# Kernel optimization log

Hardware: AMD Instinct MI355X
Metric: run time of the kernel (lower is better)

## Reference

```python
import jax, jax.numpy as jnp
import numpy as np
from jax import lax

N = 512  # neurons (== input features in this base class)

@jax.custom_vjp
def spike_fn(x):
    # Heaviside spike with fast-sigmoid surrogate gradient (standard for LIF SNNs)
    return (x > 0.0).astype(x.dtype)

def _spike_fwd(x):
    return spike_fn(x), x

def _spike_bwd(x, g):
    sg = 1.0 / (1.0 + 10.0 * jnp.abs(x)) ** 2
    return (g * sg,)

spike_fn.defvjp(_spike_fwd, _spike_bwd)

def setup_inputs() -> dict:
    key = jax.random.key(0)
    k1, k2, k3, k4, k5, k6 = jax.random.split(key, 6)
    B, T = 64, 1000
    scale = 1.0 / np.sqrt(N)
    return {
        "input_batch": jax.random.normal(k1, (B, T, N), dtype=jnp.float32),
        "state_snn": jnp.zeros((2, B, N), dtype=jnp.float32),  # [v; s]
        "state_LI": jnp.zeros((B, N), dtype=jnp.float32),
        "W1": jax.random.normal(k2, (N, N), dtype=jnp.float32) * scale,
        "W2": jax.random.normal(k3, (N, N), dtype=jnp.float32) * scale,
        "leak_v": jax.random.uniform(k4, (N,), dtype=jnp.float32, minval=0.8, maxval=0.99),
        "leak_i": jax.random.uniform(k5, (N,), dtype=jnp.float32, minval=0.8, maxval=0.99),
        "thresh": jax.random.uniform(k6, (N,), dtype=jnp.float32, minval=0.5, maxval=1.5),
    }

def reference(input_batch, state_snn, state_LI, W1, W2, leak_v, leak_i, thresh):
    # input_batch: [B, T, N]; time loop expressed as lax.scan over T
    v0, s0 = state_snn[0], state_snn[1]
    xs = jnp.swapaxes(input_batch, 0, 1)  # [T, B, N]

    def step(carry, x_t):
        v, s, u = carry
        ff = x_t @ W1.T                        # LIF feed-forward current
        v = leak_v * v * (1.0 - s) + ff        # leak + reset-to-zero on spike
        s = spike_fn(v - thresh)               # spike generation
        u = leak_i * u + s @ W2.T              # leaky-integrator readout
        return (v, s, u), (s, jnp.stack([v, s]), u)

    _, (spikes, states_snn, decoded) = lax.scan(step, (v0, s0, state_LI), xs)
    # spikes: [T,B,N], states_snn: [T,2,B,N], decoded: [T,B,N]
    return spikes, states_snn, decoded
```

## Files before the change

### kernel.cpp

```cpp
#include <hip/hip_runtime.h>

#define T_STEPS 1000
#define B_SZ 64
#define N_SZ 512
#define BN_TOT (B_SZ * N_SZ)
#define TBN   ((size_t)T_STEPS * BN_TOT)

typedef __attribute__((ext_vector_type(4))) float f32x4;
typedef __attribute__((ext_vector_type(8))) short bf16x8;
typedef unsigned short ushort_t;

__global__ __launch_bounds__(256, 4)
void sgemm_abt(const float* __restrict__ A, const float* __restrict__ W,
               float* __restrict__ C)
{
    constexpr int K = 512;
    constexpr int BK = 16;
    constexpr int LDT = 128 + 4;
    __shared__ float As[BK][LDT];
    __shared__ float Bs[BK][LDT];

    const int tid = threadIdx.x;
    const int tx = tid & 15;
    const int ty = tid >> 4;
    const size_t m0 = (size_t)blockIdx.y * 128;
    const int n0 = blockIdx.x * 128;

    float acc[8][8];
#pragma unroll
    for (int i = 0; i < 8; ++i)
#pragma unroll
        for (int j = 0; j < 8; ++j) acc[i][j] = 0.0f;

    for (int k0 = 0; k0 < K; k0 += BK) {
#pragma unroll
        for (int p = 0; p < 2; ++p) {
            int i = tid + p * 256;
            int r = i >> 2;
            int q = i & 3;
            float4 va = *(const float4*)(A + (m0 + r) * K + k0 + q * 4);
            As[q * 4 + 0][r] = va.x; As[q * 4 + 1][r] = va.y;
            As[q * 4 + 2][r] = va.z; As[q * 4 + 3][r] = va.w;
            float4 vb = *(const float4*)(W + (size_t)(n0 + r) * K + k0 + q * 4);
            Bs[q * 4 + 0][r] = vb.x; Bs[q * 4 + 1][r] = vb.y;
            Bs[q * 4 + 2][r] = vb.z; Bs[q * 4 + 3][r] = vb.w;
        }
        __syncthreads();
#pragma unroll
        for (int k = 0; k < BK; ++k) {
            float a[8], b[8];
            *(float4*)&a[0] = *(const float4*)&As[k][ty * 8];
            *(float4*)&a[4] = *(const float4*)&As[k][ty * 8 + 4];
            *(float4*)&b[0] = *(const float4*)&Bs[k][tx * 4];
            *(float4*)&b[4] = *(const float4*)&Bs[k][tx * 4 + 64];
#pragma unroll
            for (int i = 0; i < 8; ++i)
#pragma unroll
                for (int j = 0; j < 8; ++j)
                    acc[i][j] = fmaf(a[i], b[j], acc[i][j]);
        }
        __syncthreads();
    }

#pragma unroll
    for (int i = 0; i < 8; ++i) {
        float* cp = C + (m0 + ty * 8 + i) * 512 + n0 + tx * 4;
        *(float4*)cp        = make_float4(acc[i][0], acc[i][1], acc[i][2], acc[i][3]);
        *(float4*)(cp + 64) = make_float4(acc[i][4], acc[i][5], acc[i][6], acc[i][7]);
    }
}

__global__ __launch_bounds__(256)
void w2_split(const float* __restrict__ W2, ushort_t* __restrict__ Wc)
{
    int i = blockIdx.x * 256 + threadIdx.x;
    int n = i >> 9, k = i & 511;
    float w = W2[i];
    unsigned wb = __float_as_uint(w);
    float h = __uint_as_float(wb & 0xFFFF0000u);
    float r1 = w - h;
    unsigned r1b = __float_as_uint(r1);
    size_t base = (size_t)n * 1024 + k;
    Wc[base]       = (ushort_t)(wb >> 16);
    Wc[base + 512] = (ushort_t)(r1b >> 16);
}

__global__ __launch_bounds__(256, 2)
void gemm2_mfma(const ushort_t* __restrict__ S, const ushort_t* __restrict__ Wc,
                float* __restrict__ C)
{
    constexpr int NT = 1024 / 32;
    __shared__ ushort_t As[2][128 * 32];
    __shared__ ushort_t Bs[2][128 * 32];

    const int tid = threadIdx.x;
    const int m0 = blockIdx.y * 128;
    const int n0 = blockIdx.x * 128;
    const int wid = tid >> 6;
    const int lane = tid & 63;
    const int wm = (wid >> 1) * 64;
    const int wn = (wid & 1) * 64;
    const int fr = lane & 15;
    const int fq = lane >> 4;

    f32x4 acc[4][4] = {};

    const int rA = tid >> 2;
    const int cA = (tid & 3) * 8;

#define STAGE(buf, t)                                                        \
    {                                                                        \
        const int k0_ = (t) * 32;                                            \
        const int kk_ = k0_ & 511;         \
        _Pragma("unroll")                                                    \
        for (int i = 0; i < 2; ++i) {                                        \
            __builtin_amdgcn_global_load_lds(                                \
                (const __attribute__((address_space(1))) unsigned int*)      \
                    (S + (size_t)(m0 + i * 64 + rA) * 512 + kk_ + cA),       \
                (__attribute__((address_space(3))) unsigned int*)            \
                    (As[buf] + i * 2048 + tid * 8),                          \
                16, 0, 0);                                                   \
            __builtin_amdgcn_global_load_lds(                                \
                (const __attribute__((address_space(1))) unsigned int*)      \
                    (Wc + (size_t)(n0 + i * 64 + rA) * 1024 + k0_ + cA),     \
                (__attribute__((address_space(3))) unsigned int*)            \
                    (Bs[buf] + i * 2048 + tid * 8),                          \
                16, 0, 0);                                                   \
        }                                                                    \
    }

    STAGE(0, 0);
    asm volatile("s_waitcnt vmcnt(0)" ::: "memory");
    __syncthreads();

    int cur = 0;
    for (int t = 0; t < NT; ++t) {
        if (t + 1 < NT)
            STAGE(cur ^ 1, t + 1);

        bf16x8 a[4], b[4];
#pragma unroll
        for (int m = 0; m < 4; ++m)
            a[m] = *(const bf16x8*)(As[cur] + (wm + m * 16 + fr) * 32 + fq * 8);
#pragma unroll
        for (int n = 0; n < 4; ++n)
            b[n] = *(const bf16x8*)(Bs[cur] + (wn + n * 16 + fr) * 32 + fq * 8);
#pragma unroll
        for (int m = 0; m < 4; ++m)
#pragma unroll
            for (int n = 0; n < 4; ++n)
                acc[m][n] = __builtin_amdgcn_mfma_f32_16x16x32_bf16(
                    a[m], b[n], acc[m][n], 0, 0, 0);

        asm volatile("s_waitcnt vmcnt(0)" ::: "memory");
        __syncthreads();
        cur ^= 1;
    }
#undef STAGE

#pragma unroll
    for (int m = 0; m < 4; ++m) {
        const int row = m0 + wm + m * 16 + fq * 4;
#pragma unroll
        for (int n = 0; n < 4; ++n) {
            const int col = n0 + wn + n * 16 + fr;
#pragma unroll
            for (int j = 0; j < 4; ++j)
                C[(size_t)(row + j) * 512 + col] = acc[m][n][j];
        }
    }
}

__global__ __launch_bounds__(128)
void lif_scan(const float* __restrict__ ff, const float* __restrict__ st0,
              const float* __restrict__ leak_v, const float* __restrict__ thresh,
              float* __restrict__ spikes, float* __restrict__ states,
              ushort_t* __restrict__ sbf)
{
    const int idx = blockIdx.x * 128 + threadIdx.x;
    const int n = idx & (N_SZ - 1);
    const int b = idx >> 9;

    float v = st0[idx];
    float s = st0[BN_TOT + idx];
    const float lv = leak_v[n];
    const float th = thresh[n];

    const float* fp = ff + (size_t)b * T_STEPS * N_SZ + n;
    float* sp  = spikes + idx;
    float* stp = states + idx;
    ushort_t* sbp = sbf ? (sbf + idx) : (ushort_t*)0;

    float f0 = fp[0], f1 = fp[N_SZ], f2 = fp[2 * N_SZ], f3 = fp[3 * N_SZ];

    for (int t = 0; t < T_STEPS; t += 4) {
        float g0 = 0.f, g1 = 0.f, g2 = 0.f, g3 = 0.f;
        if (t + 4 < T_STEPS) {
            const float* q = fp + (size_t)(t + 4) * N_SZ;
            g0 = q[0]; g1 = q[N_SZ]; g2 = q[2 * N_SZ]; g3 = q[3 * N_SZ];
        }
#define LIF_STEP(F, TOFF)                                                  \
        {                                                                  \
            v = lv * v * (1.0f - s) + (F);                                 \
            s = (v > th) ? 1.0f : 0.0f;                                    \
            size_t o  = (size_t)(t + (TOFF)) * BN_TOT;                     \
            size_t o2 = (size_t)(t + (TOFF)) * (2 * BN_TOT);               \
            sp[o] = s;                                                     \
            stp[o2] = v;                                                   \
            stp[o2 + BN_TOT] = s;                                          \
            if (sbp) sbp[o] = (ushort_t)(__float_as_uint(s) >> 16);        \
        }
        LIF_STEP(f0, 0) LIF_STEP(f1, 1) LIF_STEP(f2, 2) LIF_STEP(f3, 3)
#undef LIF_STEP
        f0 = g0; f1 = g1; f2 = g2; f3 = g3;
    }
}

__global__ __launch_bounds__(128)
void li_scan(float* __restrict__ dec, const float* __restrict__ u0,
             const float* __restrict__ leak_i)
{
    const int idx = blockIdx.x * 128 + threadIdx.x;
    const int n = idx & (N_SZ - 1);

    float u = u0[idx];
    const float li = leak_i[n];
    float* p = dec + idx;

    float y0 = p[0], y1 = p[BN_TOT], y2 = p[2 * (size_t)BN_TOT], y3 = p[3 * (size_t)BN_TOT];

    for (int t = 0; t < T_STEPS; t += 4) {
        float g0 = 0.f, g1 = 0.f, g2 = 0.f, g3 = 0.f;
        if (t + 4 < T_STEPS) {
            float* q = p + (size_t)(t + 4) * BN_TOT;
            g0 = q[0]; g1 = q[BN_TOT]; g2 = q[2 * (size_t)BN_TOT]; g3 = q[3 * (size_t)BN_TOT];
        }
#define LI_STEP(Y, TOFF)                                                   \
        {                                                                  \
            u = fmaf(li, u, (Y));                                          \
            p[(size_t)(t + (TOFF)) * BN_TOT] = u;                          \
        }
        LI_STEP(y0, 0) LI_STEP(y1, 1) LI_STEP(y2, 2) LI_STEP(y3, 3)
#undef LI_STEP
        y0 = g0; y1 = g1; y2 = g2; y3 = g3;
    }
}

extern "C" void kernel_launch(void* const* d_in, const int* in_sizes, int n_in,
                              void* d_out, int out_size, void* d_ws, size_t ws_size,
                              hipStream_t stream)
{
    (void)in_sizes; (void)n_in; (void)out_size;

    const float* X     = (const float*)d_in[0];
    const float* st_sn = (const float*)d_in[1];
    const float* st_li = (const float*)d_in[2];
    const float* W1    = (const float*)d_in[3];
    const float* W2    = (const float*)d_in[4];
    const float* lv    = (const float*)d_in[5];
    const float* li    = (const float*)d_in[6];
    const float* th    = (const float*)d_in[7];

    float* spikes = (float*)d_out;
    float* states = spikes + TBN;
    float* dec    = states + 2 * TBN;

    const size_t WS_NEED = (size_t)512 * 1024 * 2 + (size_t)64000 * 512 * 2;
    const bool use_mfma = (ws_size >= WS_NEED);
    ushort_t* Wc = (ushort_t*)d_ws;
    ushort_t* Sb = Wc + (size_t)512 * 1024;

    const dim3 gemm_grid(4, 500), gemm_block(256);
    const dim3 scan_grid(BN_TOT / 128), scan_block(128);

    if (use_mfma)
        w2_split<<<dim3(1024), dim3(256), 0, stream>>>(W2, Wc);

    sgemm_abt<<<gemm_grid, gemm_block, 0, stream>>>(X, W1, dec);

    lif_scan<<<scan_grid, scan_block, 0, stream>>>(dec, st_sn, lv, th,
                                                   spikes, states,
                                                   use_mfma ? Sb : (ushort_t*)0);

    if (use_mfma)
        gemm2_mfma<<<gemm_grid, gemm_block, 0, stream>>>(Sb, Wc, dec);
    else
        sgemm_abt<<<gemm_grid, gemm_block, 0, stream>>>(spikes, W2, dec);

    li_scan<<<scan_grid, scan_block, 0, stream>>>(dec, st_li, li);
}
```

Before: 811.8 us.

## Pack spikes into ballot bitmasks and expand to bf16 in GEMM2 staging

The LIF scan no longer writes a per-element bf16 spike array. Instead it uses a wave ballot to write one 64-bit spike bitmask per wave per timestep. The MFMA GEMM reads these masks and expands each bit into a bf16 1.0/0 pair (high and low K halves) in registers, then stores that into shared memory in place of the async global-to-LDS copy of A. Both scans are also unrolled from 4 to 8 timesteps with deeper prefetch. This cuts the spike intermediate traffic about 16x, at the cost of ALU work, a ballot per step and synchronous LDS stores in the GEMM loop.

After: 732.3 us. -9.8%, faster.

```diff
diff --git a/kernel.cpp b/kernel.cpp
--- a/kernel.cpp
+++ b/kernel.cpp
@@ -85,8 +85,18 @@
     Wc[base + 512] = (ushort_t)(r1b >> 16);
 }
 
+__device__ __forceinline__ uint4 mexp8(unsigned bb)
+{
+    uint4 r;
+    r.x = ((bb) & 1u) * 0x3F80u        | (((bb) >> 1) & 1u) * 0x3F800000u;
+    r.y = (((bb) >> 2) & 1u) * 0x3F80u | (((bb) >> 3) & 1u) * 0x3F800000u;
+    r.z = (((bb) >> 4) & 1u) * 0x3F80u | (((bb) >> 5) & 1u) * 0x3F800000u;
+    r.w = (((bb) >> 6) & 1u) * 0x3F80u | (((bb) >> 7) & 1u) * 0x3F800000u;
+    return r;
+}
+
 __global__ __launch_bounds__(256, 2)
-void gemm2_mfma(const ushort_t* __restrict__ S, const ushort_t* __restrict__ Wc,
+void gemm2_mfma(const unsigned* __restrict__ Msk, const ushort_t* __restrict__ Wc,
                 float* __restrict__ C)
 {
     constexpr int NT = 1024 / 32;
@@ -107,19 +117,17 @@
 
     const int rA = tid >> 2;
     const int cA = (tid & 3) * 8;
-
-#define STAGE(buf, t)                                                        \
+    const size_t mrow0 = (size_t)(m0 + (tid >> 2)) * 16;
+    const size_t mrow1 = (size_t)(m0 + 64 + (tid >> 2)) * 16;
+    const int qsh = (tid & 3) * 8;
+
+    unsigned mw0, mw1;
+
+#define STAGE_B(buf, t)                                                      \
     {                                                                        \
         const int k0_ = (t) * 32;                                            \
-        const int kk_ = k0_ & 511;         \
         _Pragma("unroll")                                                    \
         for (int i = 0; i < 2; ++i) {                                        \
-            __builtin_amdgcn_global_load_lds(                                \
-                (const __attribute__((address_space(1))) unsigned int*)      \
-                    (S + (size_t)(m0 + i * 64 + rA) * 512 + kk_ + cA),       \
-                (__attribute__((address_space(3))) unsigned int*)            \
-                    (As[buf] + i * 2048 + tid * 8),                          \
-                16, 0, 0);                                                   \
             __builtin_amdgcn_global_load_lds(                                \
                 (const __attribute__((address_space(1))) unsigned int*)      \
                     (Wc + (size_t)(n0 + i * 64 + rA) * 1024 + k0_ + cA),     \
@@ -128,15 +136,30 @@
                 16, 0, 0);                                                   \
         }                                                                    \
     }
-
-    STAGE(0, 0);
+#define MLOAD(t)                                                             \
+    {                                                                        \
+        const int kk_ = ((t) * 32) & 511;       \
+        mw0 = Msk[mrow0 + (kk_ >> 5)];                                       \
+        mw1 = Msk[mrow1 + (kk_ >> 5)];                                       \
+    }
+#define MSTORE(buf)                                                          \
+    {                                                                        \
+        *(uint4*)(As[buf] + tid * 8)        = mexp8((mw0 >> qsh) & 0xFFu);   \
+        *(uint4*)(As[buf] + 2048 + tid * 8) = mexp8((mw1 >> qsh) & 0xFFu);   \
+    }
+
+    MLOAD(0);
+    STAGE_B(0, 0);
+    MSTORE(0);
     asm volatile("s_waitcnt vmcnt(0)" ::: "memory");
     __syncthreads();
 
     int cur = 0;
     for (int t = 0; t < NT; ++t) {
-        if (t + 1 < NT)
-            STAGE(cur ^ 1, t + 1);
+        if (t + 1 < NT) {
+            MLOAD(t + 1);
+            STAGE_B(cur ^ 1, t + 1);
+        }
 
         bf16x8 a[4], b[4];
 #pragma unroll
@@ -152,11 +175,16 @@
                 acc[m][n] = __builtin_amdgcn_mfma_f32_16x16x32_bf16(
                     a[m], b[n], acc[m][n], 0, 0, 0);
 
+        if (t + 1 < NT)
+            MSTORE(cur ^ 1);
+
         asm volatile("s_waitcnt vmcnt(0)" ::: "memory");
         __syncthreads();
         cur ^= 1;
     }
-#undef STAGE
+#undef STAGE_B
+#undef MLOAD
+#undef MSTORE
 
 #pragma unroll
     for (int m = 0; m < 4; ++m) {
@@ -175,7 +203,7 @@
 void lif_scan(const float* __restrict__ ff, const float* __restrict__ st0,
               const float* __restrict__ leak_v, const float* __restrict__ thresh,
               float* __restrict__ spikes, float* __restrict__ states,
-              ushort_t* __restrict__ sbf)
+              unsigned long long* __restrict__ Msk)
 {
     const int idx = blockIdx.x * 128 + threadIdx.x;
     const int n = idx & (N_SZ - 1);
@@ -189,30 +217,37 @@
     const float* fp = ff + (size_t)b * T_STEPS * N_SZ + n;
     float* sp  = spikes + idx;
     float* stp = states + idx;
-    ushort_t* sbp = sbf ? (sbf + idx) : (ushort_t*)0;
-
-    float f0 = fp[0], f1 = fp[N_SZ], f2 = fp[2 * N_SZ], f3 = fp[3 * N_SZ];
-
-    for (int t = 0; t < T_STEPS; t += 4) {
-        float g0 = 0.f, g1 = 0.f, g2 = 0.f, g3 = 0.f;
-        if (t + 4 < T_STEPS) {
-            const float* q = fp + (size_t)(t + 4) * N_SZ;
-            g0 = q[0]; g1 = q[N_SZ]; g2 = q[2 * N_SZ]; g3 = q[3 * N_SZ];
-        }
-#define LIF_STEP(F, TOFF)                                                  \
-        {                                                                  \
-            v = lv * v * (1.0f - s) + (F);                                 \
-            s = (v > th) ? 1.0f : 0.0f;                                    \
-            size_t o  = (size_t)(t + (TOFF)) * BN_TOT;                     \
-            size_t o2 = (size_t)(t + (TOFF)) * (2 * BN_TOT);               \
-            sp[o] = s;                                                     \
-            stp[o2] = v;                                                   \
-            stp[o2 + BN_TOT] = s;                                          \
-            if (sbp) sbp[o] = (ushort_t)(__float_as_uint(s) >> 16);        \
-        }
-        LIF_STEP(f0, 0) LIF_STEP(f1, 1) LIF_STEP(f2, 2) LIF_STEP(f3, 3)
-#undef LIF_STEP
-        f0 = g0; f1 = g1; f2 = g2; f3 = g3;
+    const int wslot = idx >> 6;
+    const bool wlead = ((threadIdx.x & 63) == 0);
+
+    float f[8];
+#pragma unroll
+    for (int j = 0; j < 8; ++j) f[j] = fp[(size_t)j * N_SZ];
+
+    for (int t = 0; t < T_STEPS; t += 8) {
+        float g[8];
+#pragma unroll
+        for (int j = 0; j < 8; ++j) g[j] = 0.f;
+        if (t + 8 < T_STEPS) {
+            const float* q = fp + (size_t)(t + 8) * N_SZ;
+#pragma unroll
+            for (int j = 0; j < 8; ++j) g[j] = q[(size_t)j * N_SZ];
+        }
+#pragma unroll
+        for (int j = 0; j < 8; ++j) {
+            v = lv * v * (1.0f - s) + f[j];
+            s = (v > th) ? 1.0f : 0.0f;
+            size_t o  = (size_t)(t + j) * BN_TOT;
+            size_t o2 = (size_t)(t + j) * (2 * BN_TOT);
+            sp[o] = s;
+            stp[o2] = v;
+            stp[o2 + BN_TOT] = s;
+            unsigned long long bm = __ballot(s != 0.0f);
+            if (Msk && wlead)
+                Msk[(size_t)(t + j) * 512 + wslot] = bm;
+        }
+#pragma unroll
+        for (int j = 0; j < 8; ++j) f[j] = g[j];
     }
 }
 
@@ -227,22 +262,26 @@
     const float li = leak_i[n];
     float* p = dec + idx;
 
-    float y0 = p[0], y1 = p[BN_TOT], y2 = p[2 * (size_t)BN_TOT], y3 = p[3 * (size_t)BN_TOT];
-
-    for (int t = 0; t < T_STEPS; t += 4) {
-        float g0 = 0.f, g1 = 0.f, g2 = 0.f, g3 = 0.f;
-        if (t + 4 < T_STEPS) {
-            float* q = p + (size_t)(t + 4) * BN_TOT;
-            g0 = q[0]; g1 = q[BN_TOT]; g2 = q[2 * (size_t)BN_TOT]; g3 = q[3 * (size_t)BN_TOT];
-        }
-#define LI_STEP(Y, TOFF)                                                   \
-        {                                                                  \
-            u = fmaf(li, u, (Y));                                          \
-            p[(size_t)(t + (TOFF)) * BN_TOT] = u;                          \
-        }
-        LI_STEP(y0, 0) LI_STEP(y1, 1) LI_STEP(y2, 2) LI_STEP(y3, 3)
-#undef LI_STEP
-        y0 = g0; y1 = g1; y2 = g2; y3 = g3;
+    float y[8];
+#pragma unroll
+    for (int j = 0; j < 8; ++j) y[j] = p[(size_t)j * BN_TOT];
+
+    for (int t = 0; t < T_STEPS; t += 8) {
+        float g[8];
+#pragma unroll
+        for (int j = 0; j < 8; ++j) g[j] = 0.f;
+        if (t + 8 < T_STEPS) {
+            float* q = p + (size_t)(t + 8) * BN_TOT;
+#pragma unroll
+            for (int j = 0; j < 8; ++j) g[j] = q[(size_t)j * BN_TOT];
+        }
+#pragma unroll
+        for (int j = 0; j < 8; ++j) {
+            u = fmaf(li, u, y[j]);
+            p[(size_t)(t + j) * BN_TOT] = u;
+        }
+#pragma unroll
+        for (int j = 0; j < 8; ++j) y[j] = g[j];
     }
 }
 
@@ -265,10 +304,10 @@
     float* states = spikes + TBN;
     float* dec    = states + 2 * TBN;
 
-    const size_t WS_NEED = (size_t)512 * 1024 * 2 + (size_t)64000 * 512 * 2;
+    const size_t WS_NEED = (size_t)512 * 1024 * 2 + (size_t)1000 * 512 * 8;
     const bool use_mfma = (ws_size >= WS_NEED);
     ushort_t* Wc = (ushort_t*)d_ws;
-    ushort_t* Sb = Wc + (size_t)512 * 1024;
+    unsigned long long* Msk = (unsigned long long*)(Wc + (size_t)512 * 1024);
 
     const dim3 gemm_grid(4, 500), gemm_block(256);
     const dim3 scan_grid(BN_TOT / 128), scan_block(128);
@@ -280,10 +319,12 @@
 
     lif_scan<<<scan_grid, scan_block, 0, stream>>>(dec, st_sn, lv, th,
                                                    spikes, states,
-                                                   use_mfma ? Sb : (ushort_t*)0);
+                                                   use_mfma ? Msk
+                                                            : (unsigned long long*)0);
 
     if (use_mfma)
-        gemm2_mfma<<<gemm_grid, gemm_block, 0, stream>>>(Sb, Wc, dec);
+        gemm2_mfma<<<gemm_grid, gemm_block, 0, stream>>>((const unsigned*)Msk,
+                                                         Wc, dec);
     else
         sgemm_abt<<<gemm_grid, gemm_block, 0, stream>>>(spikes, W2, dec);
 
```
